# Performance work log

Hardware: AMD Instinct MI355X
Metric: run time of the kernel (lower is better)

## Reference

```python
import jax, jax.numpy as jnp
import numpy as np

KEEP_RATIO = 0.5
GROUP_RATIO = 0.5
TOPK = 2


def setup_inputs() -> dict:
    key = jax.random.key(0)
    k1, k2 = jax.random.split(key)
    tk = jax.random.normal(k1, (64, 577, 768), dtype=jnp.float32)
    # attention-map style input: strictly positive (softmax probabilities)
    attention = jax.random.uniform(k2, (64, 577, 576), dtype=jnp.float32)
    return {"tk": tk, "attention": attention}


def _take_rows(x, idx):
    # x: [B, T, ...], idx: [B, G] -> gather along axis 1 (torch index_select helper)
    return jnp.take_along_axis(x, idx.reshape(idx.shape + (1,) * (x.ndim - 2)), axis=1)


def _aggregate(x, dense_adj, k):
    """KthAverageAggregator on a dense per-image adjacency.
    x: [B, S, D] node features, dense_adj: [B, S, S] similarity (edge i->j is [b,i,j]).
    Returns aggregated features [B,S,D] and in-degree [B,S] (self loops excluded)."""
    B, S, _ = dense_adj.shape
    eye = jnp.eye(S, dtype=dense_adj.dtype)
    adj = dense_adj * (1.0 - eye)                      # zero diagonal
    topk_idx = jax.lax.top_k(adj, k)[1]                # [B, S, k]
    binary = jnp.max(jax.nn.one_hot(topk_idx, S, dtype=adj.dtype), axis=2)  # scatter 1s
    binary = ((binary + jnp.swapaxes(binary, 1, 2)) > 0).astype(adj.dtype)  # symmetrize
    W = adj * binary                                   # weighted kept edges
    M = W != 0                                         # edge mask (dense_to_sparse keeps nonzeros)

    Wsg = jax.lax.stop_gradient(W)                     # mask selection is non-differentiable

    def step(m):
        mf = m.astype(Wsg.dtype)
        deg = mf.sum(axis=1)                           # in-degree of dst j: sum over src i
        s = (Wsg * mf).sum(axis=1)                     # index_add_ of attrs at dst
        avg = jnp.where(deg > 0, s / jnp.where(deg > 0, deg, 1.0), 0.0)
        # keep edge i->j iff avg_sim[j] > avg_sim[i]
        return m & (avg[:, None, :] > avg[:, :, None])

    def cond_fun(c):
        prev, m = c
        return jnp.sum(m, dtype=jnp.int32) != prev

    def body_fun(c):
        prev, m = c
        return (jnp.sum(m, dtype=jnp.int32), step(m))

    _, m = jax.lax.while_loop(cond_fun, body_fun, (jnp.array(-1, jnp.int32), M))

    Wf = W * m.astype(W.dtype)
    # propagate with aggr='sum', message = x_j * edge_weight; self loops have weight 1
    out = jnp.einsum('bij,bid->bjd', Wf, x) + x
    deg = m.sum(axis=1).astype(jnp.float32)            # in-degree after filtering, no self loops
    return out, deg


def reference(tk, attention):
    B, N, D = tk.shape
    P = N - 1
    cls_tk, tokens = tk[:, :1], tk[:, 1:]
    cls_attn = attention[:, 0, :]                      # [B, P]
    order = jnp.argsort(-cls_attn, axis=1)             # descending sort index
    x = _take_rows(tokens, order)                      # [B, P, D] sorted patch tokens
    # reorder attention: rows 1.. by order, then all P columns by order
    rows = jnp.concatenate([attention[:, :1], _take_rows(attention[:, 1:], order)], axis=1)
    A = jnp.take_along_axis(rows, order[:, None, :], axis=2)   # [B, N, P]

    density = int(P * KEEP_RATIO)
    S = P - density
    non_skip, skip = x[:, :density], x[:, density:]
    skip_attn = A[:, density + 1:, density:]           # [B, S, S]

    skip_embs, deg = _aggregate(skip, skip_attn, TOPK)

    G = int(S * GROUP_RATIO)
    group_idx = jax.lax.top_k(deg, G)[1]               # [B, G] highest-degree skip nodes
    skip_sel = _take_rows(skip_embs, group_idx)        # [B, G, D]

    # regroup attention rows then columns, then crop
    A1 = jnp.concatenate([A[:, :density + 1], _take_rows(A[:, density + 1:], group_idx)], axis=1)
    cols = jnp.take_along_axis(A1[:, :, density:], group_idx[:, None, :], axis=2)
    R = jnp.concatenate([A1[:, :, :density], cols], axis=2)   # [B, density+G+1, density+G]

    out_tokens = jnp.concatenate([cls_tk, non_skip, skip_sel], axis=1)
    return out_tokens, R
```

## Files before the change

kernel.cpp:

```cpp
#include <hip/hip_runtime.h>
#include <math.h>


#define BATCH 64
#define NTOK 577
#define PTOK 576
#define DIM 768
#define DENS 288
#define SSZ 288
#define GSZ 144
#define MAXE 1152
#define AB_STRIDE (NTOK*PTOK)
#define TK_BSTRIDE (NTOK*DIM)
#define OUT_ROWS 433
#define R_COLS 432
#define OUT_TOK_TOTAL ((size_t)BATCH*OUT_ROWS*DIM)
#define WS_NEEDED ((size_t)995584)

__global__ __launch_bounds__(PTOK) void k_sort(const float* __restrict__ attn,
                                               int* __restrict__ order) {
  __shared__ float v[PTOK];
  const int b = blockIdx.x;
  const int t = threadIdx.x;
  v[t] = attn[(size_t)b * AB_STRIDE + t];
  __syncthreads();
  const float vi = v[t];
  int rank = 0;
  #pragma unroll 4
  for (int j = 0; j < PTOK; ++j) {
    const float vj = v[j];
    rank += ((vj > vi) || (vj == vi && j < t)) ? 1 : 0;
  }
  order[b * PTOK + rank] = t;
}

__global__ __launch_bounds__(256) void k_top2(const float* __restrict__ attn,
                                              const int* __restrict__ order,
                                              int* __restrict__ t2a,
                                              int* __restrict__ t2b) {
  const int rowg = blockIdx.x * 4 + (threadIdx.x >> 6);
  const int lane = threadIdx.x & 63;
  const int b = rowg / SSZ;
  const int i = rowg - b * SSZ;
  const int* ordb = order + b * PTOK + DENS;
  const float* arow = attn + (size_t)b * AB_STRIDE + (size_t)(1 + ordb[i]) * PTOK;

  float v1 = -1.0f, v2 = -1.0f;
  int i1 = 1 << 30, i2 = 1 << 30;
  for (int j = lane; j < SSZ; j += 64) {
    const float v = (j == i) ? 0.0f : arow[ordb[j]];
    if (v > v1) { v2 = v1; i2 = i1; v1 = v; i1 = j; }
    else if (v > v2) { v2 = v; i2 = j; }
  }
  for (int m = 1; m < 64; m <<= 1) {
    const float o1 = __shfl_xor(v1, m); const int oi1 = __shfl_xor(i1, m);
    const float o2 = __shfl_xor(v2, m); const int oi2 = __shfl_xor(i2, m);
    const bool aFirst = (v1 > o1) || (v1 == o1 && i1 < oi1);
    float nv1, nv2; int ni1, ni2;
    if (aFirst) {
      nv1 = v1; ni1 = i1;
      const bool s = (v2 > o1) || (v2 == o1 && i2 < oi1);
      nv2 = s ? v2 : o1; ni2 = s ? i2 : oi1;
    } else {
      nv1 = o1; ni1 = oi1;
      const bool s = (o2 > v1) || (o2 == v1 && oi2 < i1);
      nv2 = s ? o2 : v1; ni2 = s ? oi2 : i1;
    }
    v1 = nv1; i1 = ni1; v2 = nv2; i2 = ni2;
  }
  if (lane == 0) { t2a[rowg] = i1; t2b[rowg] = i2; }
}

__global__ __launch_bounds__(SSZ) void k_graph(const float* __restrict__ attn,
                                               const int* __restrict__ order,
                                               const int* __restrict__ t2a,
                                               const int* __restrict__ t2b,
                                               int* __restrict__ gidx,
                                               int* __restrict__ cs_g,
                                               int* __restrict__ eidx_g,
                                               float* __restrict__ ew_g) {
  __shared__ unsigned colbits[SSZ * 9];
  __shared__ int scan[SSZ];
  __shared__ int col_start[SSZ + 1];
  __shared__ int eidx[MAXE];
  __shared__ float ew[MAXE];
  __shared__ float avg[SSZ];
  __shared__ int degc[SSZ];
  __shared__ int s_changed;
  const int b = blockIdx.x;
  const int t = threadIdx.x;

  for (int k = t; k < SSZ * 9; k += SSZ) colbits[k] = 0;
  __syncthreads();

  const int rb = b * SSZ;
  const int a1 = t2a[rb + t], a2 = t2b[rb + t];
  atomicOr(&colbits[a1 * 9 + (t >> 5)], 1u << (t & 31));
  atomicOr(&colbits[a2 * 9 + (t >> 5)], 1u << (t & 31));
  atomicOr(&colbits[t * 9 + (a1 >> 5)], 1u << (a1 & 31));
  atomicOr(&colbits[t * 9 + (a2 >> 5)], 1u << (a2 & 31));
  __syncthreads();

  int cnt = 0;
  #pragma unroll
  for (int k = 0; k < 9; ++k) cnt += __popc(colbits[t * 9 + k]);
  scan[t] = cnt;
  __syncthreads();
  for (int off = 1; off < SSZ; off <<= 1) {
    const int v = (t >= off) ? scan[t - off] : 0;
    __syncthreads();
    scan[t] += v;
    __syncthreads();
  }
  if (t == 0) col_start[0] = 0;
  col_start[t + 1] = scan[t];
  __syncthreads();

  {
    const int* ordb = order + b * PTOK + DENS;
    const float* ab = attn + (size_t)b * AB_STRIDE;
    const int cj = ordb[t];
    int p = col_start[t];
    #pragma unroll
    for (int k = 0; k < 9; ++k) {
      unsigned m = colbits[t * 9 + k];
      while (m) {
        const int bit = __ffs(m) - 1; m &= m - 1;
        const int i = k * 32 + bit;
        const float w = (i == t) ? 0.0f
                                 : ab[(size_t)(1 + ordb[i]) * PTOK + cj];
        eidx[p] = i; ew[p] = w; ++p;
      }
    }
  }
  __syncthreads();

  for (;;) {
    if (t == 0) s_changed = 0;
    {
      const int s0 = col_start[t], s1 = col_start[t + 1];
      float ss = 0.0f; int dd = 0;
      for (int p = s0; p < s1; ++p) {
        const float w = ew[p];
        ss += w; dd += (w != 0.0f) ? 1 : 0;
      }
      degc[t] = dd;
      avg[t] = (dd > 0) ? (ss / (float)dd) : 0.0f;
    }
    __syncthreads();
    {
      const int s0 = col_start[t], s1 = col_start[t + 1];
      int local = 0;
      const float aj = avg[t];
      for (int p = s0; p < s1; ++p) {
        if (ew[p] != 0.0f && !(aj > avg[eidx[p]])) { ew[p] = 0.0f; local = 1; }
      }
      if (local) s_changed = 1;
    }
    __syncthreads();
    const int ch = s_changed;
    __syncthreads();
    if (ch == 0) break;
  }

  {
    const int dj = degc[t];
    int rank = 0;
    for (int j2 = 0; j2 < SSZ; ++j2) {
      const int d2 = degc[j2];
      rank += ((d2 > dj) || (d2 == dj && j2 < t)) ? 1 : 0;
    }
    if (rank < GSZ) gidx[b * GSZ + rank] = t;
  }

  for (int k = t; k < SSZ + 1; k += SSZ) cs_g[b * (SSZ + 1) + k] = col_start[k];
  const int E = col_start[SSZ];
  for (int k = t; k < E; k += SSZ) {
    eidx_g[b * MAXE + k] = eidx[k];
    ew_g[b * MAXE + k] = ew[k];
  }
}

__global__ __launch_bounds__(192) void k_out_tokens(const float* __restrict__ tk,
                                                    const int* __restrict__ order,
                                                    const int* __restrict__ gidx,
                                                    const int* __restrict__ cs_g,
                                                    const int* __restrict__ eidx_g,
                                                    const float* __restrict__ ew_g,
                                                    float* __restrict__ out) {
  const int r = blockIdx.x;
  const int b = blockIdx.y;
  const int t = threadIdx.x;
  const float* tkb = tk + (size_t)b * TK_BSTRIDE;
  float4 res;
  if (r == 0) {
    res = ((const float4*)tkb)[t];
  } else if (r <= DENS) {
    const int srow = 1 + order[b * PTOK + (r - 1)];
    res = ((const float4*)(tkb + (size_t)srow * DIM))[t];
  } else {
    const int j = gidx[b * GSZ + (r - (DENS + 1))];
    const int* ordb = order + b * PTOK + DENS;
    const int s0 = cs_g[b * (SSZ + 1) + j];
    const int s1 = cs_g[b * (SSZ + 1) + j + 1];
    const float4 xj = ((const float4*)(tkb + (size_t)(1 + ordb[j]) * DIM))[t];
    float4 acc = make_float4(0.f, 0.f, 0.f, 0.f);
    for (int p = s0; p < s1; ++p) {
      const float w = ew_g[b * MAXE + p];
      if (w != 0.0f) {
        const int i = eidx_g[b * MAXE + p];
        const float4 xv = ((const float4*)(tkb + (size_t)(1 + ordb[i]) * DIM))[t];
        acc.x += w * xv.x; acc.y += w * xv.y;
        acc.z += w * xv.z; acc.w += w * xv.w;
      }
    }
    res = make_float4(acc.x + xj.x, acc.y + xj.y, acc.z + xj.z, acc.w + xj.w);
  }
  ((float4*)(out + ((size_t)b * OUT_ROWS + r) * DIM))[t] = res;
}

__global__ __launch_bounds__(PTOK) void k_R(const float* __restrict__ attn,
                                            const int* __restrict__ order,
                                            const int* __restrict__ gidx,
                                            float* __restrict__ outR) {
  __shared__ float rowbuf[PTOK];
  const int r = blockIdx.x;
  const int b = blockIdx.y;
  const int t = threadIdx.x;
  const int arow = (r <= DENS) ? r : (DENS + 1) + gidx[b * GSZ + (r - (DENS + 1))];
  const int srcrow = (arow == 0) ? 0 : 1 + order[b * PTOK + (arow - 1)];
  rowbuf[t] = attn[(size_t)b * AB_STRIDE + (size_t)srcrow * PTOK + t];
  __syncthreads();
  if (t < R_COLS) {
    const int acol = (t < DENS) ? t : DENS + gidx[b * GSZ + (t - DENS)];
    outR[((size_t)b * OUT_ROWS + r) * R_COLS + t] = rowbuf[order[b * PTOK + acol]];
  }
}

extern "C" void kernel_launch(void* const* d_in, const int* in_sizes, int n_in,
                              void* d_out, int out_size, void* d_ws, size_t ws_size,
                              hipStream_t stream) {
  if (ws_size < WS_NEEDED) return;

  const float* tk   = (const float*)d_in[0];
  const float* attn = (const float*)d_in[1];
  float* out = (float*)d_out;

  char* ws = (char*)d_ws;
  int*   order = (int*)(ws);
  int*   t2a   = (int*)(ws + 147456);
  int*   t2b   = (int*)(ws + 221184);
  int*   gidx  = (int*)(ws + 294912);
  int*   cs    = (int*)(ws + 331776);
  int*   eidx  = (int*)(ws + 405760);
  float* ew    = (float*)(ws + 700672);

  k_sort<<<BATCH, PTOK, 0, stream>>>(attn, order);
  k_top2<<<(BATCH * SSZ) / 4, 256, 0, stream>>>(attn, order, t2a, t2b);
  k_graph<<<BATCH, SSZ, 0, stream>>>(attn, order, t2a, t2b, gidx, cs, eidx, ew);
  k_out_tokens<<<dim3(OUT_ROWS, BATCH), 192, 0, stream>>>(tk, order, gidx,
                                                          cs, eidx, ew, out);
  k_R<<<dim3(OUT_ROWS, BATCH), PTOK, 0, stream>>>(attn, order, gidx,
                                                  out + OUT_TOK_TOTAL);
}
```

Before: 385.8 us.

## Run iterative edge-pruning loop in a single wavefront without block barriers

Moves the fixed-point edge-pruning loop of the graph kernel from all 288 threads to a single 64-lane wavefront. This replaces block-wide __syncthreads and the shared change flag with wave barriers and a ballot. Edge work is now spread evenly over a flat edge list, using a new per-edge column array, instead of per-column loops. The intent is to cut barrier overhead per iteration. The cost is fewer active lanes doing the per-iteration work, plus extra shared memory for the column array.

```diff
diff --git a/kernel.cpp b/kernel.cpp
--- a/kernel.cpp
+++ b/kernel.cpp
@@ -83,10 +83,10 @@
   __shared__ int scan[SSZ];
   __shared__ int col_start[SSZ + 1];
   __shared__ int eidx[MAXE];
+  __shared__ int ecol[MAXE];
   __shared__ float ew[MAXE];
   __shared__ float avg[SSZ];
   __shared__ int degc[SSZ];
-  __shared__ int s_changed;
   const int b = blockIdx.x;
   const int t = threadIdx.x;
 
@@ -129,39 +129,40 @@
         const int i = k * 32 + bit;
         const float w = (i == t) ? 0.0f
                                  : ab[(size_t)(1 + ordb[i]) * PTOK + cj];
-        eidx[p] = i; ew[p] = w; ++p;
-      }
-    }
-  }
-  __syncthreads();
-
-  for (;;) {
-    if (t == 0) s_changed = 0;
-    {
-      const int s0 = col_start[t], s1 = col_start[t + 1];
-      float ss = 0.0f; int dd = 0;
-      for (int p = s0; p < s1; ++p) {
-        const float w = ew[p];
-        ss += w; dd += (w != 0.0f) ? 1 : 0;
-      }
-      degc[t] = dd;
-      avg[t] = (dd > 0) ? (ss / (float)dd) : 0.0f;
-    }
-    __syncthreads();
-    {
-      const int s0 = col_start[t], s1 = col_start[t + 1];
-      int local = 0;
-      const float aj = avg[t];
-      for (int p = s0; p < s1; ++p) {
-        if (ew[p] != 0.0f && !(aj > avg[eidx[p]])) { ew[p] = 0.0f; local = 1; }
-      }
-      if (local) s_changed = 1;
-    }
-    __syncthreads();
-    const int ch = s_changed;
-    __syncthreads();
-    if (ch == 0) break;
-  }
+        eidx[p] = i; ecol[p] = t; ew[p] = w; ++p;
+      }
+    }
+  }
+  __syncthreads();
+
+  if (t < 64) {
+    const int E = col_start[SSZ];
+    for (;;) {
+      for (int j = t; j < SSZ; j += 64) {
+        const int s0 = col_start[j], s1 = col_start[j + 1];
+        float ss = 0.0f; int dd = 0;
+        for (int p = s0; p < s1; ++p) {
+          const float w = ew[p];
+          ss += w; dd += (w != 0.0f) ? 1 : 0;
+        }
+        degc[j] = dd;
+        avg[j] = (dd > 0) ? (ss / (float)dd) : 0.0f;
+      }
+      __builtin_amdgcn_wave_barrier();
+      asm volatile("" ::: "memory");
+      bool changed = false;
+      for (int e = t; e < E; e += 64) {
+        const float w = ew[e];
+        if (w != 0.0f && !(avg[ecol[e]] > avg[eidx[e]])) {
+          ew[e] = 0.0f; changed = true;
+        }
+      }
+      __builtin_amdgcn_wave_barrier();
+      asm volatile("" ::: "memory");
+      if (__ballot(changed) == 0ull) break;
+    }
+  }
+  __syncthreads();
 
   {
     const int dj = degc[t];
```

Measured after the change: 408.7 us. +5.9%, slower.
